# Optimization experiments

Measured on AMD Instinct MI355X. Metric: run time of the kernel, lower is better.

Reference implementation:

```python
import jax, jax.numpy as jnp
import numpy as np

N_NODES = 100000
N_EDGES = 1600000
D_IN = 128
D_HID = 128
D_OUT = 64
N_GRAPHS = 128


def setup_inputs() -> dict:
    key = jax.random.key(0)
    ks = jax.random.split(key, 8)
    x = jax.random.normal(ks[0], (N_NODES, D_IN), dtype=jnp.float32)
    edge_index = jax.random.randint(ks[1], (2, N_EDGES), 0, N_NODES, dtype=jnp.int64)
    batch = jnp.sort(jax.random.randint(ks[2], (N_NODES,), 0, N_GRAPHS, dtype=jnp.int64))
    def glorot(k, fi, fo):
        s = jnp.sqrt(6.0 / (fi + fo)).astype(jnp.float32)
        return jax.random.uniform(k, (fi, fo), jnp.float32, -1.0, 1.0) * s
    return {
        "x": x, "edge_index": edge_index, "batch": batch,
        "W1": glorot(ks[3], D_IN, D_HID), "b1": jnp.zeros((D_HID,), jnp.float32),
        "W2": glorot(ks[4], D_HID, D_HID), "b2": jnp.zeros((D_HID,), jnp.float32),
        "W3": glorot(ks[5], D_HID, D_HID), "b3": jnp.zeros((D_HID,), jnp.float32),
        "Wfc": glorot(ks[6], D_HID, D_OUT), "bfc": jnp.zeros((D_OUT,), jnp.float32),
    }


def _gcn_graph(edge_index, n_nodes):
    # add self-loops and compute symmetric normalization (PyG gcn_norm)
    loop = jnp.arange(n_nodes, dtype=edge_index.dtype)
    src = jnp.concatenate([edge_index[0], loop])
    dst = jnp.concatenate([edge_index[1], loop])
    deg = jax.ops.segment_sum(jnp.ones_like(dst, dtype=jnp.float32), dst,
                              num_segments=n_nodes)
    dinv = jnp.where(deg > 0, jax.lax.rsqrt(deg), 0.0)
    norm = dinv[src] * dinv[dst]  # [E + N]
    return src, dst, norm


def _gcn_conv(x, src, dst, norm, W, b, n_nodes):
    h = x @ W                                    # [N, F_out]
    msg = h[src] * norm[:, None]                 # gather + scale
    agg = jax.ops.segment_sum(msg, dst, num_segments=n_nodes)  # scatter-add
    return agg + b


def reference(x, edge_index, batch, W1, b1, W2, b2, W3, b3, Wfc, bfc):
    n = x.shape[0]
    src, dst, norm = _gcn_graph(edge_index, n)
    h = jax.nn.relu(_gcn_conv(x, src, dst, norm, W1, b1, n))
    h = jax.nn.relu(_gcn_conv(h, src, dst, norm, W2, b2, n))
    h = jax.nn.relu(_gcn_conv(h, src, dst, norm, W3, b3, n))
    # global mean pool over graphs in the batch
    sums = jax.ops.segment_sum(h, batch, num_segments=N_GRAPHS)
    cnts = jax.ops.segment_sum(jnp.ones((n,), jnp.float32), batch,
                               num_segments=N_GRAPHS)
    pooled = sums / jnp.maximum(cnts, 1.0)[:, None]   # [G, D_HID]
    return pooled @ Wfc + bfc                         # [G, D_OUT]
```

## Files before the change

kernel.cpp:

```cpp
#include <hip/hip_runtime.h>

#define NN 100000
#define NE 1600000
#define DF 128
#define DOUT 64
#define NG 128
#define NB 391
#define EPB 8192
#define NBLKA ((NE + EPB - 1) / EPB)
#define NBLKX 6250
#define PCH 8

typedef short short8 __attribute__((ext_vector_type(8)));
typedef float floatx4 __attribute__((ext_vector_type(4)));
typedef float floatx2 __attribute__((ext_vector_type(2)));

__device__ __forceinline__ unsigned short f2bf(float f) {
    unsigned int b = __float_as_uint(f);
    unsigned int r = (b + 0x7fffu + ((b >> 16) & 1u)) >> 16;
    return (unsigned short)r;
}
__device__ __forceinline__ float bf2f_lo(unsigned int v) { return __uint_as_float(v << 16); }
__device__ __forceinline__ float bf2f_hi(unsigned int v) { return __uint_as_float(v & 0xffff0000u); }

__device__ __forceinline__ int phi(int p) {
    return (((p >> 6) << 2) + (p & 3)) * 16 + ((p >> 2) & 15);
}


__global__ __launch_bounds__(256) void k_init(int* __restrict__ bhist,
                                              const int* __restrict__ batch,
                                              int* __restrict__ gstart,
                                              const float* __restrict__ W1,
                                              const float* __restrict__ W2,
                                              const float* __restrict__ W3,
                                              unsigned short* __restrict__ O1,
                                              unsigned short* __restrict__ O2,
                                              unsigned short* __restrict__ O3) {
    int blk = blockIdx.x;
    if (blk < 2) {
        int i = blk * 256 + threadIdx.x;
        if (i < NB) bhist[i] = 0;
    } else if (blk == 2) {
        int g = threadIdx.x;
        if (g > NG) return;
        int lo = 0, hi = NN;
        while (lo < hi) {
            int mid = (lo + hi) >> 1;
            if (batch[mid] < g) lo = mid + 1; else hi = mid;
        }
        gstart[g] = lo;
    } else {
        int bb = blk - 3;
        const float* W = (bb >= 16) ? W3 : (bb >= 8) ? W2 : W1;
        unsigned short* O = (bb >= 16) ? O3 : (bb >= 8) ? O2 : O1;
        int idx = (bb & 7) * 256 + threadIdx.x;
        int l = idx & 63;
        int s = (idx >> 6) & 3;
        int tt = idx >> 8;
        int k0 = s * 32 + (l >> 4) * 8;
        int c = tt * 16 + (l & 15);
        unsigned short o[8];
#pragma unroll
        for (int j = 0; j < 8; j++) o[j] = f2bf(W[phi(k0 + j) * DF + c]);
        *(short8*)&O[idx * 8] = *(short8*)o;
    }
}


__global__ __launch_bounds__(256) void k_pre(const int* __restrict__ dst,
                                             int* __restrict__ bhist,
                                             const float* __restrict__ x,
                                             unsigned short* __restrict__ xb) {
    __shared__ int lh[NB];
    int t = threadIdx.x;
    if (blockIdx.x < NBLKA) {
        for (int i = t; i < NB; i += 256) lh[i] = 0;
        __syncthreads();
        int e0 = blockIdx.x * EPB;
        int e1 = min(e0 + EPB, NE);
        for (int e = e0 + t; e < e1; e += 256) atomicAdd(&lh[dst[e] >> 8], 1);
        __syncthreads();
        for (int i = t; i < NB; i += 256) {
            int c = lh[i];
            if (c) atomicAdd(&bhist[i], c);
        }
    } else {
        size_t i = ((size_t)(blockIdx.x - NBLKA) * 256 + t) * 8;
        size_t rb = i & ~(size_t)127;
        int p0 = (int)(i & 127);
        unsigned short o[8];
#pragma unroll
        for (int j = 0; j < 8; j++) o[j] = f2bf(x[rb + phi(p0 + j)]);
        *(short8*)&xb[i] = *(short8*)o;
    }
}

__global__ __launch_bounds__(512) void k_bscan(const int* __restrict__ bhist,
                                               int* __restrict__ bbase,
                                               int* __restrict__ bcur) {
    __shared__ int sh[512];
    int t = threadIdx.x;
    int v = (t < NB) ? bhist[t] : 0;
    sh[t] = v;
    __syncthreads();
    for (int off = 1; off < 512; off <<= 1) {
        int a = (t >= off) ? sh[t - off] : 0;
        __syncthreads();
        sh[t] += a;
        __syncthreads();
    }
    if (t < NB) {
        bbase[t] = sh[t] - v;
        bcur[t] = sh[t] - v;
    }
    if (t == NB - 1) bbase[NB] = sh[t];
}

__global__ __launch_bounds__(256) void k_pairs(const int* __restrict__ src,
                                               const int* __restrict__ dst,
                                               int* __restrict__ bcur,
                                               int2* __restrict__ ebuf) {
    __shared__ int lh[NB];
    __shared__ int lbase[NB];
    int t = threadIdx.x;
    for (int i = t; i < NB; i += 256) lh[i] = 0;
    __syncthreads();
    int e0 = blockIdx.x * EPB;
    int e1 = min(e0 + EPB, NE);
    for (int e = e0 + t; e < e1; e += 256) atomicAdd(&lh[dst[e] >> 8], 1);
    __syncthreads();
    for (int i = t; i < NB; i += 256) {
        int c = lh[i];
        lbase[i] = c ? atomicAdd(&bcur[i], c) : 0;
    }
    __syncthreads();
    for (int i = t; i < NB; i += 256) lh[i] = 0;
    __syncthreads();
    for (int e = e0 + t; e < e1; e += 256) {
        int s = src[e], d = dst[e];
        int bk = d >> 8;
        int off = atomicAdd(&lh[bk], 1);
        ebuf[lbase[bk] + off] = make_int2(s, d);
    }
}

__global__ __launch_bounds__(256) void k_build(const int2* __restrict__ ebuf,
                                               const int* __restrict__ bbase,
                                               int* __restrict__ rowptr,
                                               float* __restrict__ dinv,
                                               int* __restrict__ col) {
    __shared__ int deg[256];
    __shared__ int lst[256];
    int b = blockIdx.x, t = threadIdx.x;
    int n0 = b << 8;
    int node = n0 + t;
    deg[t] = 0;
    __syncthreads();
    int e0 = bbase[b], e1 = bbase[b + 1];
    for (int e = e0 + t; e < e1; e += 256) atomicAdd(&deg[ebuf[e].y - n0], 1);
    __syncthreads();
    int v = deg[t];
    lst[t] = v;
    __syncthreads();
    for (int off = 1; off < 256; off <<= 1) {
        int a = (t >= off) ? lst[t - off] : 0;
        __syncthreads();
        lst[t] += a;
        __syncthreads();
    }
    int mystart = e0 + lst[t] - v;
    if (node < NN) {
        rowptr[node] = mystart;
        dinv[node] = rsqrtf((float)(v + 1));
    }
    if (b == NB - 1 && t == 255) rowptr[NN] = e1;
    lst[t] = mystart;
    __syncthreads();
    for (int e = e0 + t; e < e1; e += 256) {
        int2 pr = ebuf[e];
        int p = atomicAdd(&lst[pr.y - n0], 1);
        col[p] = pr.x * DF;
    }
}


__global__ __launch_bounds__(256) void k_gemm(const unsigned short* __restrict__ X,
                                              const unsigned short* __restrict__ Wb,
                                              const float* __restrict__ dinv,
                                              unsigned char* __restrict__ fs8) {
    int t = threadIdx.x;
    int wave = t >> 6, l = t & 63;
    int r0 = blockIdx.x * 64 + wave * 16;
    int lm = l & 15, q = l >> 4;

    int arow = r0 + lm;
    if (arow >= NN) arow = NN - 1;
    const unsigned short* xrow = X + (size_t)arow * DF + q * 8;
    short8 af0 = *(const short8*)(xrow);
    short8 af1 = *(const short8*)(xrow + 32);
    short8 af2 = *(const short8*)(xrow + 64);
    short8 af3 = *(const short8*)(xrow + 96);

    int orow = r0 + q * 4;
    float dv[4];
#pragma unroll
    for (int j = 0; j < 4; j++) dv[j] = (orow + j < NN) ? dinv[orow + j] : 0.f;

    float res[4][8];
#pragma unroll
    for (int tt = 0; tt < 8; tt++) {
        floatx4 acc = {0.f, 0.f, 0.f, 0.f};
        const unsigned short* wp = Wb + ((size_t)(tt * 4) * 64 + l) * 8;
        acc = __builtin_amdgcn_mfma_f32_16x16x32_bf16(af0, *(const short8*)(wp), acc, 0, 0, 0);
        acc = __builtin_amdgcn_mfma_f32_16x16x32_bf16(af1, *(const short8*)(wp + 512), acc, 0, 0, 0);
        acc = __builtin_amdgcn_mfma_f32_16x16x32_bf16(af2, *(const short8*)(wp + 1024), acc, 0, 0, 0);
        acc = __builtin_amdgcn_mfma_f32_16x16x32_bf16(af3, *(const short8*)(wp + 1536), acc, 0, 0, 0);
#pragma unroll
        for (int j = 0; j < 4; j++) res[j][tt] = acc[j] * dv[j];
    }

#pragma unroll
    for (int g = 0; g < 2; g++) {
#pragma unroll
        for (int j = 0; j < 4; j++) {
            int r = orow + j;
            if (r >= NN) continue;
            unsigned int w8 = __builtin_amdgcn_cvt_pk_fp8_f32(res[j][g * 4 + 0], res[j][g * 4 + 1], 0, false);
            w8 = __builtin_amdgcn_cvt_pk_fp8_f32(res[j][g * 4 + 2], res[j][g * 4 + 3], w8, true);
            *(unsigned int*)&fs8[(size_t)r * DF + g * 64 + lm * 4] = w8;
        }
    }
}

__global__ __launch_bounds__(256) void k_agg(const unsigned char* __restrict__ fs8,
                                             const int* __restrict__ colb,
                                             const int* __restrict__ rowptr,
                                             const float* __restrict__ dinv,
                                             const float* __restrict__ b,
                                             unsigned short* __restrict__ out) {
    int n = (int)((blockIdx.x * (size_t)blockDim.x + threadIdx.x) >> 6);
    int lane = threadIdx.x & 63;
    int sub = lane >> 4;
    int fo = lane & 15;
    int foff = fo * 8;

    int e0 = rowptr[n], e1 = rowptr[n + 1];
    int degn = e1 - e0;

    floatx2 acc0 = {0.f, 0.f}, acc1 = {0.f, 0.f}, acc2 = {0.f, 0.f}, acc3 = {0.f, 0.f};

    if (degn > 16) {
        for (int base = e0; base < e1; base += 32) {
            int idx[8], cb[8];
#pragma unroll
            for (int k = 0; k < 8; k++) {
                idx[k] = base + k * 4 + sub;
                cb[k] = colb[min(idx[k], e1 - 1)];
            }
            uint2 vv[8];
#pragma unroll
            for (int k = 0; k < 8; k++) vv[k] = *(const uint2*)&fs8[(size_t)cb[k] + foff];
#pragma unroll
            for (int k = 0; k < 8; k++) {
                if (idx[k] < e1) {
                    acc0 += __builtin_amdgcn_cvt_pk_f32_fp8(vv[k].x, false);
                    acc1 += __builtin_amdgcn_cvt_pk_f32_fp8(vv[k].x, true);
                    acc2 += __builtin_amdgcn_cvt_pk_f32_fp8(vv[k].y, false);
                    acc3 += __builtin_amdgcn_cvt_pk_f32_fp8(vv[k].y, true);
                }
            }
        }
    } else if (degn > 0) {
        int idx[4], cb[4];
#pragma unroll
        for (int k = 0; k < 4; k++) {
            idx[k] = e0 + k * 4 + sub;
            cb[k] = colb[min(idx[k], e1 - 1)];
        }
        uint2 vv[4];
#pragma unroll
        for (int k = 0; k < 4; k++) vv[k] = *(const uint2*)&fs8[(size_t)cb[k] + foff];
#pragma unroll
        for (int k = 0; k < 4; k++) {
            if (idx[k] < e1) {
                acc0 += __builtin_amdgcn_cvt_pk_f32_fp8(vv[k].x, false);
                acc1 += __builtin_amdgcn_cvt_pk_f32_fp8(vv[k].x, true);
                acc2 += __builtin_amdgcn_cvt_pk_f32_fp8(vv[k].y, false);
                acc3 += __builtin_amdgcn_cvt_pk_f32_fp8(vv[k].y, true);
            }
        }
    }

    float a[8] = {acc0.x, acc0.y, acc1.x, acc1.y, acc2.x, acc2.y, acc3.x, acc3.y};
#pragma unroll
    for (int j = 0; j < 8; j++) {
        a[j] += __shfl_xor(a[j], 16);
        a[j] += __shfl_xor(a[j], 32);
    }

    if (sub == 0) {
        uint2 sv = *(const uint2*)&fs8[(size_t)n * DF + foff];
        floatx2 s0 = __builtin_amdgcn_cvt_pk_f32_fp8(sv.x, false);
        floatx2 s1 = __builtin_amdgcn_cvt_pk_f32_fp8(sv.x, true);
        floatx2 s2 = __builtin_amdgcn_cvt_pk_f32_fp8(sv.y, false);
        floatx2 s3 = __builtin_amdgcn_cvt_pk_f32_fp8(sv.y, true);
        float sf[8] = {s0.x, s0.y, s1.x, s1.y, s2.x, s2.y, s3.x, s3.y};
        float dvn = dinv[n];
        float o[8];
#pragma unroll
        for (int j = 0; j < 8; j++)
            o[j] = fmaxf(dvn * (a[j] + sf[j]) + b[phi(foff + j)], 0.f);
        uint4 pk;
        pk.x = (unsigned int)f2bf(o[0]) | ((unsigned int)f2bf(o[1]) << 16);
        pk.y = (unsigned int)f2bf(o[2]) | ((unsigned int)f2bf(o[3]) << 16);
        pk.z = (unsigned int)f2bf(o[4]) | ((unsigned int)f2bf(o[5]) << 16);
        pk.w = (unsigned int)f2bf(o[6]) | ((unsigned int)f2bf(o[7]) << 16);
        *(uint4*)&out[(size_t)n * DF + foff] = pk;
    }
}


__global__ __launch_bounds__(256) void k_poolA(const unsigned short* __restrict__ h,
                                               const int* __restrict__ gstart,
                                               float* __restrict__ part) {
    __shared__ float2 red[256];
    int g = blockIdx.x >> 3, c = blockIdx.x & 7;
    int s = gstart[g], e = gstart[g + 1];
    int len = e - s;
    int cs = s + (int)(((long long)len * c) >> 3);
    int ce = s + (int)(((long long)len * (c + 1)) >> 3);
    int t = threadIdx.x;
    int fp = t & 63;
    int rs = t >> 6;
    float2 acc = make_float2(0.f, 0.f);
    for (int n = cs + rs; n < ce; n += 4) {
        unsigned int v = *(const unsigned int*)&h[(size_t)n * DF + fp * 2];
        acc.x += bf2f_lo(v);
        acc.y += bf2f_hi(v);
    }
    red[t] = acc;
    __syncthreads();
    if (rs == 0) {
        float2 a0 = red[fp], a1 = red[fp + 64], a2 = red[fp + 128], a3 = red[fp + 192];
        float2 o;
        o.x = (a0.x + a1.x) + (a2.x + a3.x);
        o.y = (a0.y + a1.y) + (a2.y + a3.y);
        *(float2*)&part[(size_t)blockIdx.x * DF + fp * 2] = o;
    }
}

__global__ __launch_bounds__(128) void k_poolfc(const float* __restrict__ part,
                                                const int* __restrict__ gstart,
                                                const float* __restrict__ Wfc,
                                                const float* __restrict__ bfc,
                                                float* __restrict__ out) {
    __shared__ float pl[DF];
    int g = blockIdx.x;
    int f = threadIdx.x;
    float s = 0.f;
#pragma unroll
    for (int c = 0; c < PCH; c++) s += part[(size_t)(g * PCH + c) * DF + f];
    int cnt = gstart[g + 1] - gstart[g];
    pl[phi(f)] = s / (float)max(cnt, 1);
    __syncthreads();
    if (f < DOUT) {
        float acc = bfc[f];
        for (int k = 0; k < DF; k++) acc += pl[k] * Wfc[k * DOUT + f];
        out[g * DOUT + f] = acc;
    }
}


extern "C" void kernel_launch(void* const* d_in, const int* in_sizes, int n_in,
                              void* d_out, int out_size, void* d_ws, size_t ws_size,
                              hipStream_t stream) {
    const float* x     = (const float*)d_in[0];
    const int*   ei    = (const int*)d_in[1];
    const int*   batch = (const int*)d_in[2];
    const float* W1 = (const float*)d_in[3];
    const float* b1 = (const float*)d_in[4];
    const float* W2 = (const float*)d_in[5];
    const float* b2 = (const float*)d_in[6];
    const float* W3 = (const float*)d_in[7];
    const float* b3 = (const float*)d_in[8];
    const float* Wfc = (const float*)d_in[9];
    const float* bfc = (const float*)d_in[10];
    float* out = (float*)d_out;

    char* p = (char*)d_ws;
    unsigned short* xb = (unsigned short*)p;  p += (size_t)NN * DF * sizeof(short);
    unsigned short* ob = (unsigned short*)p;  p += (size_t)NN * DF * sizeof(short);
    unsigned char*  fs8 = (unsigned char*)p;  p += (size_t)NN * DF;
    unsigned short* Wb1 = (unsigned short*)p; p += 16384 * sizeof(short);
    unsigned short* Wb2 = (unsigned short*)p; p += 16384 * sizeof(short);
    unsigned short* Wb3 = (unsigned short*)p; p += 16384 * sizeof(short);
    float* dinv = (float*)p;           p += (size_t)NN * sizeof(float);
    int* rowptr = (int*)p;             p += (size_t)(NN + 4) * sizeof(int);
    int* col    = (int*)p;             p += (size_t)NE * sizeof(int);
    int2* ebuf  = (int2*)p;            p += (size_t)NE * sizeof(int2);
    int* bhist  = (int*)p;             p += (size_t)(NB + 4) * sizeof(int);
    int* bbase  = (int*)p;             p += (size_t)(NB + 4) * sizeof(int);
    int* bcur   = (int*)p;             p += (size_t)(NB + 4) * sizeof(int);
    int* gstart = (int*)p;             p += (size_t)(NG + 4) * sizeof(int);
    float* part = (float*)p;           p += (size_t)NG * PCH * DF * sizeof(float);

    const int* e_src = ei;
    const int* e_dst = ei + NE;

    k_init<<<27, 256, 0, stream>>>(bhist, batch, gstart, W1, W2, W3, Wb1, Wb2, Wb3);
    k_pre<<<NBLKA + NBLKX, 256, 0, stream>>>(e_dst, bhist, x, xb);
    k_bscan<<<1, 512, 0, stream>>>(bhist, bbase, bcur);
    k_pairs<<<NBLKA, 256, 0, stream>>>(e_src, e_dst, bcur, ebuf);
    k_build<<<NB, 256, 0, stream>>>(ebuf, bbase, rowptr, dinv, col);

    int ggrid = (NN + 63) / 64;
    int agg_blocks = NN / 4;

    k_gemm<<<ggrid, 256, 0, stream>>>(xb, Wb1, dinv, fs8);
    k_agg<<<agg_blocks, 256, 0, stream>>>(fs8, col, rowptr, dinv, b1, ob);
    k_gemm<<<ggrid, 256, 0, stream>>>(ob, Wb2, dinv, fs8);
    k_agg<<<agg_blocks, 256, 0, stream>>>(fs8, col, rowptr, dinv, b2, ob);
    k_gemm<<<ggrid, 256, 0, stream>>>(ob, Wb3, dinv, fs8);
    k_agg<<<agg_blocks, 256, 0, stream>>>(fs8, col, rowptr, dinv, b3, ob);

    k_poolA<<<NG * PCH, 256, 0, stream>>>(ob, gstart, part);
    k_poolfc<<<NG, 128, 0, stream>>>(part, gstart, Wfc, bfc, out);
}
```

Measured before the change: 366.5 us.

## Map four nodes per wavefront in aggregation, dropping cross-lane reductions

The aggregation kernel now gives each 16-lane quarter of a wavefront its own node instead of splitting one node's edges across four quarters. This removes the shuffle reductions and the idle three-quarters of lanes in the epilogue, and it hoists the bias and dinv loads. The cost is load imbalance between nodes of different degree within one wave, and each quarter walks its edge list serially in chunks of 8. Separately, the edge-partition block size drops from 8192 to 2048 edges, which launches more preprocessing blocks.

Result: no change. 372.0 us (+1.5%).

```diff
diff --git a/kernel.cpp b/kernel.cpp
--- a/kernel.cpp
+++ b/kernel.cpp
@@ -6,10 +6,11 @@
 #define DOUT 64
 #define NG 128
 #define NB 391
-#define EPB 8192
+#define EPB 2048
 #define NBLKA ((NE + EPB - 1) / EPB)
 #define NBLKX 6250
 #define PCH 8
+#define NAGB (NN / 16)
 
 typedef short short8 __attribute__((ext_vector_type(8)));
 typedef float floatx4 __attribute__((ext_vector_type(4)));
@@ -239,51 +240,32 @@
                                              const float* __restrict__ dinv,
                                              const float* __restrict__ b,
                                              unsigned short* __restrict__ out) {
-    int n = (int)((blockIdx.x * (size_t)blockDim.x + threadIdx.x) >> 6);
+    int w = (int)((blockIdx.x * (size_t)blockDim.x + threadIdx.x) >> 6);
     int lane = threadIdx.x & 63;
     int sub = lane >> 4;
     int fo = lane & 15;
     int foff = fo * 8;
+    int n = w * 4 + sub;
+
+    float bias[8];
+#pragma unroll
+    for (int j = 0; j < 8; j++) bias[j] = b[phi(foff + j)];
+    float dvn = dinv[n];
 
     int e0 = rowptr[n], e1 = rowptr[n + 1];
-    int degn = e1 - e0;
 
     floatx2 acc0 = {0.f, 0.f}, acc1 = {0.f, 0.f}, acc2 = {0.f, 0.f}, acc3 = {0.f, 0.f};
 
-    if (degn > 16) {
-        for (int base = e0; base < e1; base += 32) {
-            int idx[8], cb[8];
-#pragma unroll
-            for (int k = 0; k < 8; k++) {
-                idx[k] = base + k * 4 + sub;
-                cb[k] = colb[min(idx[k], e1 - 1)];
-            }
-            uint2 vv[8];
-#pragma unroll
-            for (int k = 0; k < 8; k++) vv[k] = *(const uint2*)&fs8[(size_t)cb[k] + foff];
-#pragma unroll
-            for (int k = 0; k < 8; k++) {
-                if (idx[k] < e1) {
-                    acc0 += __builtin_amdgcn_cvt_pk_f32_fp8(vv[k].x, false);
-                    acc1 += __builtin_amdgcn_cvt_pk_f32_fp8(vv[k].x, true);
-                    acc2 += __builtin_amdgcn_cvt_pk_f32_fp8(vv[k].y, false);
-                    acc3 += __builtin_amdgcn_cvt_pk_f32_fp8(vv[k].y, true);
-                }
-            }
-        }
-    } else if (degn > 0) {
-        int idx[4], cb[4];
-#pragma unroll
-        for (int k = 0; k < 4; k++) {
-            idx[k] = e0 + k * 4 + sub;
-            cb[k] = colb[min(idx[k], e1 - 1)];
-        }
-        uint2 vv[4];
-#pragma unroll
-        for (int k = 0; k < 4; k++) vv[k] = *(const uint2*)&fs8[(size_t)cb[k] + foff];
-#pragma unroll
-        for (int k = 0; k < 4; k++) {
-            if (idx[k] < e1) {
+    for (int base = e0; base < e1; base += 8) {
+        int cb[8];
+#pragma unroll
+        for (int k = 0; k < 8; k++) cb[k] = colb[min(base + k, e1 - 1)];
+        uint2 vv[8];
+#pragma unroll
+        for (int k = 0; k < 8; k++) vv[k] = *(const uint2*)&fs8[(size_t)cb[k] + foff];
+#pragma unroll
+        for (int k = 0; k < 8; k++) {
+            if (base + k < e1) {
                 acc0 += __builtin_amdgcn_cvt_pk_f32_fp8(vv[k].x, false);
                 acc1 += __builtin_amdgcn_cvt_pk_f32_fp8(vv[k].x, true);
                 acc2 += __builtin_amdgcn_cvt_pk_f32_fp8(vv[k].y, false);
@@ -292,32 +274,22 @@
         }
     }
 
+    uint2 sv = *(const uint2*)&fs8[(size_t)n * DF + foff];
+    acc0 += __builtin_amdgcn_cvt_pk_f32_fp8(sv.x, false);
+    acc1 += __builtin_amdgcn_cvt_pk_f32_fp8(sv.x, true);
+    acc2 += __builtin_amdgcn_cvt_pk_f32_fp8(sv.y, false);
+    acc3 += __builtin_amdgcn_cvt_pk_f32_fp8(sv.y, true);
+
     float a[8] = {acc0.x, acc0.y, acc1.x, acc1.y, acc2.x, acc2.y, acc3.x, acc3.y};
-#pragma unroll
-    for (int j = 0; j < 8; j++) {
-        a[j] += __shfl_xor(a[j], 16);
-        a[j] += __shfl_xor(a[j], 32);
-    }
-
-    if (sub == 0) {
-        uint2 sv = *(const uint2*)&fs8[(size_t)n * DF + foff];
-        floatx2 s0 = __builtin_amdgcn_cvt_pk_f32_fp8(sv.x, false);
-        floatx2 s1 = __builtin_amdgcn_cvt_pk_f32_fp8(sv.x, true);
-        floatx2 s2 = __builtin_amdgcn_cvt_pk_f32_fp8(sv.y, false);
-        floatx2 s3 = __builtin_amdgcn_cvt_pk_f32_fp8(sv.y, true);
-        float sf[8] = {s0.x, s0.y, s1.x, s1.y, s2.x, s2.y, s3.x, s3.y};
-        float dvn = dinv[n];
-        float o[8];
-#pragma unroll
-        for (int j = 0; j < 8; j++)
-            o[j] = fmaxf(dvn * (a[j] + sf[j]) + b[phi(foff + j)], 0.f);
-        uint4 pk;
-        pk.x = (unsigned int)f2bf(o[0]) | ((unsigned int)f2bf(o[1]) << 16);
-        pk.y = (unsigned int)f2bf(o[2]) | ((unsigned int)f2bf(o[3]) << 16);
-        pk.z = (unsigned int)f2bf(o[4]) | ((unsigned int)f2bf(o[5]) << 16);
-        pk.w = (unsigned int)f2bf(o[6]) | ((unsigned int)f2bf(o[7]) << 16);
-        *(uint4*)&out[(size_t)n * DF + foff] = pk;
-    }
+    float o[8];
+#pragma unroll
+    for (int j = 0; j < 8; j++) o[j] = fmaxf(dvn * a[j] + bias[j], 0.f);
+    uint4 pk;
+    pk.x = (unsigned int)f2bf(o[0]) | ((unsigned int)f2bf(o[1]) << 16);
+    pk.y = (unsigned int)f2bf(o[2]) | ((unsigned int)f2bf(o[3]) << 16);
+    pk.z = (unsigned int)f2bf(o[4]) | ((unsigned int)f2bf(o[5]) << 16);
+    pk.w = (unsigned int)f2bf(o[6]) | ((unsigned int)f2bf(o[7]) << 16);
+    *(uint4*)&out[(size_t)n * DF + foff] = pk;
 }
 
 
@@ -415,14 +387,13 @@
     k_build<<<NB, 256, 0, stream>>>(ebuf, bbase, rowptr, dinv, col);
 
     int ggrid = (NN + 63) / 64;
-    int agg_blocks = NN / 4;
 
     k_gemm<<<ggrid, 256, 0, stream>>>(xb, Wb1, dinv, fs8);
-    k_agg<<<agg_blocks, 256, 0, stream>>>(fs8, col, rowptr, dinv, b1, ob);
+    k_agg<<<NAGB, 256, 0, stream>>>(fs8, col, rowptr, dinv, b1, ob);
     k_gemm<<<ggrid, 256, 0, stream>>>(ob, Wb2, dinv, fs8);
-    k_agg<<<agg_blocks, 256, 0, stream>>>(fs8, col, rowptr, dinv, b2, ob);
+    k_agg<<<NAGB, 256, 0, stream>>>(fs8, col, rowptr, dinv, b2, ob);
     k_gemm<<<ggrid, 256, 0, stream>>>(ob, Wb3, dinv, fs8);
-    k_agg<<<agg_blocks, 256, 0, stream>>>(fs8, col, rowptr, dinv, b3, ob);
+    k_agg<<<NAGB, 256, 0, stream>>>(fs8, col, rowptr, dinv, b3, ob);
 
     k_poolA<<<NG * PCH, 256, 0, stream>>>(ob, gstart, part);
     k_poolfc<<<NG, 128, 0, stream>>>(part, gstart, Wfc, bfc, out);
```
